# Performance work log

Hardware: AMD Instinct MI355X
Metric: run time of the kernel (lower is better)

## Reference

```python
import jax, jax.numpy as jnp
import numpy as np

B, S, H = 2, 2048, 1024
NH = 16
HD = H // NH


def setup_inputs() -> dict:
    key = jax.random.key(0)
    ks = jax.random.split(key, 5)
    X = jax.random.normal(ks[0], (B, S, H), dtype=jnp.float32)
    mask = jnp.ones((B, S), dtype=jnp.int32)
    W_Q = jax.random.normal(ks[1], (H, H), dtype=jnp.float32) * 0.02
    W_K = jax.random.normal(ks[2], (H, H), dtype=jnp.float32) * 0.02
    W_V = jax.random.normal(ks[3], (H, H), dtype=jnp.float32) * 0.02
    W_O = jax.random.normal(ks[4], (H, H), dtype=jnp.float32) * 0.02
    return {"X": X, "mask": mask, "W_Q": W_Q, "W_K": W_K, "W_V": W_V, "W_O": W_O}


def reference(X, mask, W_Q, W_K, W_V, W_O):
    b, s, h = X.shape
    scaling = HD ** -0.5
    # project and split heads: [b, nh, s, hd]
    Q = (X @ W_Q).reshape(b, s, NH, HD).transpose(0, 2, 1, 3)
    K = (X @ W_K).reshape(b, s, NH, HD).transpose(0, 2, 1, 3)
    V = (X @ W_V).reshape(b, s, NH, HD).transpose(0, 2, 1, 3)
    scores = jnp.einsum('bhqd,bhkd->bhqk', Q, K) * scaling
    scores = jnp.clip(scores, -10000.0, 10000.0)
    # 2D mask [b, s] -> broadcast as [b, 1, 1, s]; fill -inf where mask == 0
    m = mask[:, None, None, :]
    scores = jnp.where(m == 0, -jnp.inf, scores)
    attn = jax.nn.softmax(scores, axis=-1)
    # dropout is identity in eval / p=0
    context = jnp.einsum('bhqk,bhkd->bhqd', attn, V)
    context = context.transpose(0, 2, 1, 3).reshape(b, s, h)
    return context @ W_O
```

## Files before the change

### kernel.cpp

```cpp
#include <hip/hip_runtime.h>
#include <hip/hip_bf16.h>

#define S_LEN 2048
#define HDIM  1024
#define NHEADS 16
#define HD    64
#define QKV_STRIDE (S_LEN * 2 * HDIM)

typedef __attribute__((ext_vector_type(8))) short short8;
typedef __attribute__((ext_vector_type(4))) float float4v;

__device__ __forceinline__ unsigned short f2bf(float f) {
  return (unsigned short)((__builtin_bit_cast(unsigned int, f) + 0x8000u) >> 16);
}
__device__ __forceinline__ unsigned int pkbf(float a, float b) {
  unsigned int ua = __builtin_bit_cast(unsigned int, a) + 0x8000u;
  unsigned int ub = __builtin_bit_cast(unsigned int, b) + 0x8000u;
  return __builtin_amdgcn_perm(ub, ua, 0x07060302u);
}

__device__ __forceinline__ void async_copy16(const void* g, void* l) {
  __builtin_amdgcn_global_load_lds((__attribute__((address_space(1))) const void*)g,
                                   (__attribute__((address_space(3))) void*)l, 16, 0, 0);
}

__global__ void cast_x_kernel(const float* __restrict__ X, unsigned short* __restrict__ Xb) {
  int i = blockIdx.x * blockDim.x + threadIdx.x;
  float4 v = ((const float4*)X)[i];
  uint2 o;
  o.x = pkbf(v.x, v.y);
  o.y = pkbf(v.z, v.w);
  ((uint2*)Xb)[i] = o;
}

__global__ void trans_w_kernel(const float* __restrict__ W0, const float* __restrict__ W1,
                               const float* __restrict__ W2, const float* __restrict__ W3,
                               unsigned short* __restrict__ Wt) {
  __shared__ unsigned short tile[64][72];
  const float* W = (blockIdx.z == 0) ? W0 : (blockIdx.z == 1) ? W1 : (blockIdx.z == 2) ? W2 : W3;
  unsigned short* out = Wt + (size_t)blockIdx.z * HDIM * HDIM;
  int n0 = blockIdx.x * 64, k0 = blockIdx.y * 64;
  int t = threadIdx.x;
#pragma unroll
  for (int it = 0; it < 4; ++it) {
    int idx = it * 256 + t;
    int r  = idx >> 4;
    int c4 = (idx & 15) * 4;
    float4 v = *(const float4*)&W[(size_t)(k0 + r) * HDIM + n0 + c4];
    tile[c4 + 0][r] = f2bf(v.x);
    tile[c4 + 1][r] = f2bf(v.y);
    tile[c4 + 2][r] = f2bf(v.z);
    tile[c4 + 3][r] = f2bf(v.w);
  }
  __syncthreads();
#pragma unroll
  for (int it = 0; it < 4; ++it) {
    int idx = it * 256 + t;
    int r  = idx >> 4;
    int c4 = (idx & 15) * 4;
    ushort4 o;
    o.x = tile[r][c4 + 0]; o.y = tile[r][c4 + 1];
    o.z = tile[r][c4 + 2]; o.w = tile[r][c4 + 3];
    *(ushort4*)&out[(size_t)(n0 + r) * HDIM + k0 + c4] = o;
  }
}

__global__ __launch_bounds__(256, 3) void gemm128_kernel(
    const unsigned short* __restrict__ A,
    const unsigned short* __restrict__ B0, const unsigned short* __restrict__ B1,
    const unsigned short* __restrict__ B2,
    void* __restrict__ outp, int mode)
{
  __shared__ unsigned short sA[128 * 32];
  __shared__ unsigned short sB[128 * 32];
  const int z = blockIdx.z;
  const unsigned short* Bt = (z == 0) ? B0 : (z == 1) ? B1 : B2;
  const int m0 = blockIdx.x * 128;
  const int n0 = blockIdx.y * 128;
  const int t = threadIdx.x;
  const int lane = t & 63;
  const int w = t >> 6;
  const int wm = w & 1, wn = w >> 1;

  const int sr  = lane >> 2;
  const int scp = lane & 3;
  const int scl = scp ^ ((sr >> 1) & 3);
  const long ga0 = (long)(m0 + 16 * w + sr) * HDIM + scl * 8;
  const long ga1 = ga0 + 64l * HDIM;
  const long gb0 = (long)(n0 + 16 * w + sr) * HDIM + scl * 8;
  const long gb1 = gb0 + 64l * HDIM;
  unsigned short* lA0 = &sA[(16 * w) * 32];
  unsigned short* lA1 = &sA[(64 + 16 * w) * 32];
  unsigned short* lB0 = &sB[(16 * w) * 32];
  unsigned short* lB1 = &sB[(64 + 16 * w) * 32];

  const int fr = lane & 15;
  const int fq = lane >> 4;
  int offA[4], offB[4];
#pragma unroll
  for (int i = 0; i < 4; ++i) {
    int ra = wm * 64 + i * 16 + fr;
    offA[i] = ra * 32 + (fq ^ ((ra >> 1) & 3)) * 8;
    int rb = wn * 64 + i * 16 + fr;
    offB[i] = rb * 32 + (fq ^ ((rb >> 1) & 3)) * 8;
  }

  float4v acc[4][4] = {};

  for (int kk = 0; kk < HDIM; kk += 32) {
    __syncthreads();
    async_copy16(A + ga0 + kk, lA0);
    async_copy16(A + ga1 + kk, lA1);
    async_copy16(Bt + gb0 + kk, lB0);
    async_copy16(Bt + gb1 + kk, lB1);
    __syncthreads();
    short8 af[4], bf[4];
#pragma unroll
    for (int i = 0; i < 4; ++i) af[i] = *(const short8*)&sA[offA[i]];
#pragma unroll
    for (int i = 0; i < 4; ++i) bf[i] = *(const short8*)&sB[offB[i]];
#pragma unroll
    for (int mi = 0; mi < 4; ++mi)
#pragma unroll
      for (int ni = 0; ni < 4; ++ni)
        acc[mi][ni] = __builtin_amdgcn_mfma_f32_16x16x32_bf16(af[mi], bf[ni], acc[mi][ni], 0, 0, 0);
  }

  if (mode == 0) {
    float* out = (float*)outp;
#pragma unroll
    for (int mi = 0; mi < 4; ++mi)
#pragma unroll
      for (int ni = 0; ni < 4; ++ni)
#pragma unroll
        for (int rg = 0; rg < 4; ++rg) {
          int m = m0 + wm * 64 + mi * 16 + fq * 4 + rg;
          int n = n0 + wn * 64 + ni * 16 + fr;
          out[(size_t)m * HDIM + n] = acc[mi][ni][rg];
        }
  } else if (z != 1) {
    const float scl = (z == 0) ? 0.18033688011112042f : 1.0f;
    unsigned short* out = (unsigned short*)outp + (size_t)z * QKV_STRIDE;
#pragma unroll
    for (int mi = 0; mi < 4; ++mi)
#pragma unroll
      for (int ni = 0; ni < 4; ++ni) {
        int m = m0 + wm * 64 + mi * 16 + fq * 4;
        int n = n0 + wn * 64 + ni * 16 + fr;
        int b = m >> 11, s = m & 2047, hh = n >> 6, d = n & 63;
        uint2 pk;
        pk.x = pkbf(acc[mi][ni][0] * scl, acc[mi][ni][1] * scl);
        pk.y = pkbf(acc[mi][ni][2] * scl, acc[mi][ni][3] * scl);
        *(uint2*)&out[(((size_t)(b * NHEADS + hh)) * HD + d) * S_LEN + s] = pk;
      }
  } else {
    unsigned short* out = (unsigned short*)outp + (size_t)z * QKV_STRIDE;
#pragma unroll
    for (int mi = 0; mi < 4; ++mi)
#pragma unroll
      for (int ni = 0; ni < 4; ++ni)
#pragma unroll
        for (int rg = 0; rg < 4; ++rg) {
          int m = m0 + wm * 64 + mi * 16 + fq * 4 + rg;
          int n = n0 + wn * 64 + ni * 16 + fr;
          int b = m >> 11, s = m & 2047, hh = n >> 6, d = n & 63;
          out[(((size_t)(b * NHEADS + hh)) * S_LEN + s) * HD + d] = f2bf(acc[mi][ni][rg]);
        }
  }
}

__device__ __forceinline__ void stage_tile(char* smem, const unsigned short* Kp,
    const unsigned short* Vtp, size_t base, int tile, int w, int kr, int kc) {
  const int kv = tile * 64;
  char* bufb = smem + (tile & 1) * 16384;
  unsigned short* dK = (unsigned short*)bufb + (w * 8) * 64;
  async_copy16(Kp + base + (size_t)(kv + w * 8 + kr) * HD + ((kc ^ kr) * 8), dK);
  unsigned short* dV = (unsigned short*)(bufb + 8192) + (w * 8) * 64;
  const int d = w * 8 + kr;
  async_copy16(Vtp + base + (size_t)d * S_LEN + kv + ((kc ^ kr) * 8), dV);
}

__global__ __launch_bounds__(512, 4) void attn_kernel(
    const unsigned short* __restrict__ Qtp,
    const unsigned short* __restrict__ Kp,
    const unsigned short* __restrict__ Vtp,
    const int* __restrict__ mask,
    unsigned short* __restrict__ ctx)
{
  __shared__ __align__(16) char smem[53248];

  const int bh = blockIdx.y;
  const int b = bh >> 4;
  const int h = bh & 15;
  const size_t base = (size_t)bh * (S_LEN * HD);
  const int q0 = blockIdx.x * 128;
  const int t = threadIdx.x;
  const int lane = t & 63;
  const int w = t >> 6;
  const int qg = w >> 1;
  const int kh = w & 1;
  const int fr = lane & 15;
  const int fq = lane >> 4;
  const int kr = lane >> 3, kc = lane & 7;
  unsigned short* sPw = (unsigned short*)(smem + 32768) + w * (32 * 40);

  short8 qfr[2][2];
#pragma unroll
  for (int q_ = 0; q_ < 2; ++q_)
#pragma unroll
    for (int ks = 0; ks < 2; ++ks)
#pragma unroll
      for (int j = 0; j < 8; ++j)
        qfr[q_][ks][j] = (short)Qtp[base + (size_t)(ks * 32 + fq * 8 + j) * S_LEN
                                    + (q0 + qg * 32 + q_ * 16 + fr)];

  float l_lane[2] = {0.f, 0.f};
  float4v o_acc[4][2] = {};
  const float4v zero4 = {0.f, 0.f, 0.f, 0.f};

  int mnext = mask[b * S_LEN + lane];

  stage_tile(smem, Kp, Vtp, base, 0, w, kr, kc);

#pragma unroll 2
  for (int it = 0; it < 32; ++it) {
    __syncthreads();
    if (it < 31)
      stage_tile(smem, Kp, Vtp, base, it + 1, w, kr, kc);

    unsigned long long bal = __ballot(mnext != 0);
    if (it < 31)
      mnext = mask[b * S_LEN + (it + 1) * 64 + lane];

    const unsigned short* sKb  = (const unsigned short*)(smem + (it & 1) * 16384);
    const unsigned short* sVtb = (const unsigned short*)(smem + (it & 1) * 16384 + 8192);

    float4v s_acc[2][2];
#pragma unroll
    for (int kf = 0; kf < 2; ++kf) {
      int rk = kh * 32 + kf * 16 + fr;
      short8 k0 = *(const short8*)&sKb[rk * 64 + ((fq ^ (rk & 7)) * 8)];
      short8 k1 = *(const short8*)&sKb[rk * 64 + (((4 + fq) ^ (rk & 7)) * 8)];
#pragma unroll
      for (int q_ = 0; q_ < 2; ++q_) {
        float4v s = __builtin_amdgcn_mfma_f32_16x16x32_bf16(k0, qfr[q_][0], zero4, 0, 0, 0);
        s_acc[kf][q_] = __builtin_amdgcn_mfma_f32_16x16x32_bf16(k1, qfr[q_][1], s, 0, 0, 0);
      }
    }

    short8 vf[4];
#pragma unroll
    for (int df = 0; df < 4; ++df) {
      int rv = df * 16 + fr;
      vf[df] = *(const short8*)&sVtb[rv * 64 + (((kh * 4 + fq) ^ (fr & 7)) * 8)];
    }

#pragma unroll
    for (int kf = 0; kf < 2; ++kf) {
      unsigned mseg = 0xFu;
      if (bal != ~0ull)
        mseg = (unsigned)(bal >> (kh * 32 + kf * 16 + fq * 4)) & 0xFu;
#pragma unroll
      for (int q_ = 0; q_ < 2; ++q_) {
        float p0 = __builtin_amdgcn_exp2f(s_acc[kf][q_][0]);
        float p1 = __builtin_amdgcn_exp2f(s_acc[kf][q_][1]);
        float p2 = __builtin_amdgcn_exp2f(s_acc[kf][q_][2]);
        float p3 = __builtin_amdgcn_exp2f(s_acc[kf][q_][3]);
        if (bal != ~0ull) {
          p0 = (mseg & 1u) ? p0 : 0.f;
          p1 = (mseg & 2u) ? p1 : 0.f;
          p2 = (mseg & 4u) ? p2 : 0.f;
          p3 = (mseg & 8u) ? p3 : 0.f;
        }
        l_lane[q_] += (p0 + p1) + (p2 + p3);
        uint2 pk;
        pk.x = pkbf(p0, p1);
        pk.y = pkbf(p2, p3);
        *(uint2*)&sPw[(q_ * 16 + fr) * 40 + (kf * 4 + fq) * 4] = pk;
      }
    }

    short8 pf[2];
#pragma unroll
    for (int q_ = 0; q_ < 2; ++q_)
      pf[q_] = *(const short8*)&sPw[(q_ * 16 + fr) * 40 + fq * 8];
#pragma unroll
    for (int df = 0; df < 4; ++df)
#pragma unroll
      for (int q_ = 0; q_ < 2; ++q_)
        o_acc[df][q_] = __builtin_amdgcn_mfma_f32_16x16x32_bf16(vf[df], pf[q_], o_acc[df][q_], 0, 0, 0);
  }

#pragma unroll
  for (int q_ = 0; q_ < 2; ++q_) {
    l_lane[q_] += __shfl_xor(l_lane[q_], 16);
    l_lane[q_] += __shfl_xor(l_lane[q_], 32);
  }

  __syncthreads();
  float* red = (float*)smem;
  float* rec = red + (size_t)(qg * 64 + lane) * 34;
  if (kh) {
#pragma unroll
    for (int df = 0; df < 4; ++df)
#pragma unroll
      for (int q_ = 0; q_ < 2; ++q_) {
        int e = df * 2 + q_;
        *(float2*)&rec[4 * e]     = make_float2(o_acc[df][q_][0], o_acc[df][q_][1]);
        *(float2*)&rec[4 * e + 2] = make_float2(o_acc[df][q_][2], o_acc[df][q_][3]);
      }
    *(float2*)&rec[32] = make_float2(l_lane[0], l_lane[1]);
  }
  __syncthreads();
  if (!kh) {
#pragma unroll
    for (int df = 0; df < 4; ++df)
#pragma unroll
      for (int q_ = 0; q_ < 2; ++q_) {
        int e = df * 2 + q_;
        float2 a = *(float2*)&rec[4 * e];
        float2 c = *(float2*)&rec[4 * e + 2];
        o_acc[df][q_][0] += a.x; o_acc[df][q_][1] += a.y;
        o_acc[df][q_][2] += c.x; o_acc[df][q_][3] += c.y;
      }
    float2 lr = *(float2*)&rec[32];
    float inv_l[2];
    inv_l[0] = 1.0f / (l_lane[0] + lr.x);
    inv_l[1] = 1.0f / (l_lane[1] + lr.y);
#pragma unroll
    for (int q_ = 0; q_ < 2; ++q_) {
      size_t rowoff = ((size_t)(b * S_LEN + q0 + qg * 32 + q_ * 16 + fr)) * HDIM + h * HD;
#pragma unroll
      for (int df = 0; df < 4; ++df) {
        uint2 pk;
        pk.x = pkbf(o_acc[df][q_][0] * inv_l[q_], o_acc[df][q_][1] * inv_l[q_]);
        pk.y = pkbf(o_acc[df][q_][2] * inv_l[q_], o_acc[df][q_][3] * inv_l[q_]);
        *(uint2*)&ctx[rowoff + df * 16 + fq * 4] = pk;
      }
    }
  }
}

extern "C" void kernel_launch(void* const* d_in, const int* in_sizes, int n_in,
                              void* d_out, int out_size, void* d_ws, size_t ws_size,
                              hipStream_t stream) {
  const float* X  = (const float*)d_in[0];
  const int* mask = (const int*)d_in[1];
  const float* Wq = (const float*)d_in[2];
  const float* Wk = (const float*)d_in[3];
  const float* Wv = (const float*)d_in[4];
  const float* Wo = (const float*)d_in[5];
  float* out = (float*)d_out;

  char* ws = (char*)d_ws;
  unsigned short* Xb  = (unsigned short*)(ws);
  unsigned short* Wt  = (unsigned short*)(ws + (8u << 20));
  unsigned short* QKV = (unsigned short*)(ws + (16u << 20));
  unsigned short* CTX = (unsigned short*)(ws);

  cast_x_kernel<<<4096, 256, 0, stream>>>(X, Xb);
  trans_w_kernel<<<dim3(16, 16, 4), 256, 0, stream>>>(Wq, Wk, Wv, Wo, Wt);
  gemm128_kernel<<<dim3(32, 8, 3), 256, 0, stream>>>(
      Xb, Wt, Wt + (1u << 20), Wt + (2u << 20), QKV, 1);
  attn_kernel<<<dim3(16, 32), 512, 0, stream>>>(
      QKV, QKV + QKV_STRIDE, QKV + 2 * (size_t)QKV_STRIDE, mask, CTX);
  gemm128_kernel<<<dim3(32, 8, 1), 256, 0, stream>>>(
      CTX, Wt + (3u << 20), Wt + (3u << 20), Wt + (3u << 20), out, 0);
}
```

Measured before the change: 187.2 us.

## Merge prep kernels and fuse QKV projections into one shared-A GEMM

Folds the X cast and weight transpose into a single prep launch, removing one kernel launch. Replaces the three-way z-indexed QKV GEMM with one kernel in which each block computes a 128x64 tile for Q, K and V together. This reuses each A tile from LDS across all three weights, cutting A loads threefold. It also simplifies the output GEMM by dropping its mode branches. The cost is more accumulator registers (96 floats per lane), occupancy lowered to 2 blocks, and a grid that shrinks to 512 blocks.

```diff
diff --git a/kernel.cpp b/kernel.cpp
--- a/kernel.cpp
+++ b/kernel.cpp
@@ -24,23 +24,28 @@
                                    (__attribute__((address_space(3))) void*)l, 16, 0, 0);
 }
 
-__global__ void cast_x_kernel(const float* __restrict__ X, unsigned short* __restrict__ Xb) {
-  int i = blockIdx.x * blockDim.x + threadIdx.x;
-  float4 v = ((const float4*)X)[i];
-  uint2 o;
-  o.x = pkbf(v.x, v.y);
-  o.y = pkbf(v.z, v.w);
-  ((uint2*)Xb)[i] = o;
-}
-
-__global__ void trans_w_kernel(const float* __restrict__ W0, const float* __restrict__ W1,
-                               const float* __restrict__ W2, const float* __restrict__ W3,
-                               unsigned short* __restrict__ Wt) {
+__global__ void prep_kernel(const float* __restrict__ X, unsigned short* __restrict__ Xb,
+                            const float* __restrict__ W0, const float* __restrict__ W1,
+                            const float* __restrict__ W2, const float* __restrict__ W3,
+                            unsigned short* __restrict__ Wt) {
   __shared__ unsigned short tile[64][72];
-  const float* W = (blockIdx.z == 0) ? W0 : (blockIdx.z == 1) ? W1 : (blockIdx.z == 2) ? W2 : W3;
-  unsigned short* out = Wt + (size_t)blockIdx.z * HDIM * HDIM;
-  int n0 = blockIdx.x * 64, k0 = blockIdx.y * 64;
-  int t = threadIdx.x;
+  const int t = threadIdx.x;
+  if (blockIdx.x < 4096) {
+    int i = blockIdx.x * 256 + t;
+    float4 v = ((const float4*)X)[i];
+    uint2 o;
+    o.x = pkbf(v.x, v.y);
+    o.y = pkbf(v.z, v.w);
+    ((uint2*)Xb)[i] = o;
+    return;
+  }
+  const int wid = blockIdx.x - 4096;
+  const int z = wid >> 8;
+  const int rem = wid & 255;
+  const int n0 = (rem & 15) * 64;
+  const int k0 = (rem >> 4) * 64;
+  const float* W = (z == 0) ? W0 : (z == 1) ? W1 : (z == 2) ? W2 : W3;
+  unsigned short* out = Wt + (size_t)z * HDIM * HDIM;
 #pragma unroll
   for (int it = 0; it < 4; ++it) {
     int idx = it * 256 + t;
@@ -65,16 +70,109 @@
   }
 }
 
+__global__ __launch_bounds__(256, 2) void gemm_qkv_kernel(
+    const unsigned short* __restrict__ A,
+    const unsigned short* __restrict__ Wt,
+    unsigned short* __restrict__ out)
+{
+  __shared__ unsigned short sA[128 * 32];
+  __shared__ unsigned short sB[3 * 64 * 32];
+  const int m0 = blockIdx.x * 128;
+  const int n0 = blockIdx.y * 64;
+  const int t = threadIdx.x;
+  const int lane = t & 63;
+  const int w = t >> 6;
+  const int wm = w & 1, wn = w >> 1;
+
+  const int sr  = lane >> 2;
+  const int scp = lane & 3;
+  const int scl = scp ^ ((sr >> 1) & 3);
+  const long ga0 = (long)(m0 + 16 * w + sr) * HDIM + scl * 8;
+  const long ga1 = ga0 + 64l * HDIM;
+  const long gb  = (long)(n0 + 16 * w + sr) * HDIM + scl * 8;
+  unsigned short* lA0 = &sA[(16 * w) * 32];
+  unsigned short* lA1 = &sA[(64 + 16 * w) * 32];
+  unsigned short* lB  = &sB[(16 * w) * 32];
+
+  const int fr = lane & 15;
+  const int fq = lane >> 4;
+  int offA[4], offB[2];
+#pragma unroll
+  for (int i = 0; i < 4; ++i) {
+    int ra = wm * 64 + i * 16 + fr;
+    offA[i] = ra * 32 + (fq ^ ((ra >> 1) & 3)) * 8;
+  }
+#pragma unroll
+  for (int i = 0; i < 2; ++i) {
+    int rb = wn * 32 + i * 16 + fr;
+    offB[i] = rb * 32 + (fq ^ ((rb >> 1) & 3)) * 8;
+  }
+
+  float4v acc[3][4][2] = {};
+
+  for (int kk = 0; kk < HDIM; kk += 32) {
+    __syncthreads();
+    async_copy16(A + ga0 + kk, lA0);
+    async_copy16(A + ga1 + kk, lA1);
+#pragma unroll
+    for (int z = 0; z < 3; ++z)
+      async_copy16(Wt + (long)z * (HDIM * HDIM) + gb + kk, lB + z * 2048);
+    __syncthreads();
+    short8 af[4];
+#pragma unroll
+    for (int i = 0; i < 4; ++i) af[i] = *(const short8*)&sA[offA[i]];
+#pragma unroll
+    for (int z = 0; z < 3; ++z) {
+      short8 b0 = *(const short8*)&sB[z * 2048 + offB[0]];
+      short8 b1 = *(const short8*)&sB[z * 2048 + offB[1]];
+#pragma unroll
+      for (int mi = 0; mi < 4; ++mi) {
+        acc[z][mi][0] = __builtin_amdgcn_mfma_f32_16x16x32_bf16(af[mi], b0, acc[z][mi][0], 0, 0, 0);
+        acc[z][mi][1] = __builtin_amdgcn_mfma_f32_16x16x32_bf16(af[mi], b1, acc[z][mi][1], 0, 0, 0);
+      }
+    }
+  }
+
+#pragma unroll
+  for (int z = 0; z < 3; z += 2) {
+    const float scle = (z == 0) ? 0.18033688011112042f : 1.0f;
+    unsigned short* o = out + (size_t)z * QKV_STRIDE;
+#pragma unroll
+    for (int mi = 0; mi < 4; ++mi)
+#pragma unroll
+      for (int ni = 0; ni < 2; ++ni) {
+        int m = m0 + wm * 64 + mi * 16 + fq * 4;
+        int n = n0 + wn * 32 + ni * 16 + fr;
+        int b = m >> 11, s = m & 2047, hh = n >> 6, d = n & 63;
+        uint2 pk;
+        pk.x = pkbf(acc[z][mi][ni][0] * scle, acc[z][mi][ni][1] * scle);
+        pk.y = pkbf(acc[z][mi][ni][2] * scle, acc[z][mi][ni][3] * scle);
+        *(uint2*)&o[(((size_t)(b * NHEADS + hh)) * HD + d) * S_LEN + s] = pk;
+      }
+  }
+  {
+    unsigned short* o = out + (size_t)QKV_STRIDE;
+#pragma unroll
+    for (int mi = 0; mi < 4; ++mi)
+#pragma unroll
+      for (int ni = 0; ni < 2; ++ni)
+#pragma unroll
+        for (int rg = 0; rg < 4; ++rg) {
+          int m = m0 + wm * 64 + mi * 16 + fq * 4 + rg;
+          int n = n0 + wn * 32 + ni * 16 + fr;
+          int b = m >> 11, s = m & 2047, hh = n >> 6, d = n & 63;
+          o[(((size_t)(b * NHEADS + hh)) * S_LEN + s) * HD + d] = f2bf(acc[1][mi][ni][rg]);
+        }
+  }
+}
+
 __global__ __launch_bounds__(256, 3) void gemm128_kernel(
     const unsigned short* __restrict__ A,
-    const unsigned short* __restrict__ B0, const unsigned short* __restrict__ B1,
-    const unsigned short* __restrict__ B2,
-    void* __restrict__ outp, int mode)
+    const unsigned short* __restrict__ Bt,
+    float* __restrict__ out)
 {
   __shared__ unsigned short sA[128 * 32];
   __shared__ unsigned short sB[128 * 32];
-  const int z = blockIdx.z;
-  const unsigned short* Bt = (z == 0) ? B0 : (z == 1) ? B1 : B2;
   const int m0 = blockIdx.x * 128;
   const int n0 = blockIdx.y * 128;
   const int t = threadIdx.x;
@@ -126,47 +224,16 @@
         acc[mi][ni] = __builtin_amdgcn_mfma_f32_16x16x32_bf16(af[mi], bf[ni], acc[mi][ni], 0, 0, 0);
   }
 
-  if (mode == 0) {
-    float* out = (float*)outp;
-#pragma unroll
-    for (int mi = 0; mi < 4; ++mi)
-#pragma unroll
-      for (int ni = 0; ni < 4; ++ni)
-#pragma unroll
-        for (int rg = 0; rg < 4; ++rg) {
-          int m = m0 + wm * 64 + mi * 16 + fq * 4 + rg;
-          int n = n0 + wn * 64 + ni * 16 + fr;
-          out[(size_t)m * HDIM + n] = acc[mi][ni][rg];
-        }
-  } else if (z != 1) {
-    const float scl = (z == 0) ? 0.18033688011112042f : 1.0f;
-    unsigned short* out = (unsigned short*)outp + (size_t)z * QKV_STRIDE;
-#pragma unroll
-    for (int mi = 0; mi < 4; ++mi)
-#pragma unroll
-      for (int ni = 0; ni < 4; ++ni) {
-        int m = m0 + wm * 64 + mi * 16 + fq * 4;
+#pragma unroll
+  for (int mi = 0; mi < 4; ++mi)
+#pragma unroll
+    for (int ni = 0; ni < 4; ++ni)
+#pragma unroll
+      for (int rg = 0; rg < 4; ++rg) {
+        int m = m0 + wm * 64 + mi * 16 + fq * 4 + rg;
         int n = n0 + wn * 64 + ni * 16 + fr;
-        int b = m >> 11, s = m & 2047, hh = n >> 6, d = n & 63;
-        uint2 pk;
-        pk.x = pkbf(acc[mi][ni][0] * scl, acc[mi][ni][1] * scl);
-        pk.y = pkbf(acc[mi][ni][2] * scl, acc[mi][ni][3] * scl);
-        *(uint2*)&out[(((size_t)(b * NHEADS + hh)) * HD + d) * S_LEN + s] = pk;
-      }
-  } else {
-    unsigned short* out = (unsigned short*)outp + (size_t)z * QKV_STRIDE;
-#pragma unroll
-    for (int mi = 0; mi < 4; ++mi)
-#pragma unroll
-      for (int ni = 0; ni < 4; ++ni)
-#pragma unroll
-        for (int rg = 0; rg < 4; ++rg) {
-          int m = m0 + wm * 64 + mi * 16 + fq * 4 + rg;
-          int n = n0 + wn * 64 + ni * 16 + fr;
-          int b = m >> 11, s = m & 2047, hh = n >> 6, d = n & 63;
-          out[(((size_t)(b * NHEADS + hh)) * S_LEN + s) * HD + d] = f2bf(acc[mi][ni][rg]);
-        }
-  }
+        out[(size_t)m * HDIM + n] = acc[mi][ni][rg];
+      }
 }
 
 __device__ __forceinline__ void stage_tile(char* smem, const unsigned short* Kp,
@@ -358,12 +425,9 @@
   unsigned short* QKV = (unsigned short*)(ws + (16u << 20));
   unsigned short* CTX = (unsigned short*)(ws);
 
-  cast_x_kernel<<<4096, 256, 0, stream>>>(X, Xb);
-  trans_w_kernel<<<dim3(16, 16, 4), 256, 0, stream>>>(Wq, Wk, Wv, Wo, Wt);
-  gemm128_kernel<<<dim3(32, 8, 3), 256, 0, stream>>>(
-      Xb, Wt, Wt + (1u << 20), Wt + (2u << 20), QKV, 1);
+  prep_kernel<<<5120, 256, 0, stream>>>(X, Xb, Wq, Wk, Wv, Wo, Wt);
+  gemm_qkv_kernel<<<dim3(32, 16), 256, 0, stream>>>(Xb, Wt, QKV);
   attn_kernel<<<dim3(16, 32), 512, 0, stream>>>(
       QKV, QKV + QKV_STRIDE, QKV + 2 * (size_t)QKV_STRIDE, mask, CTX);
-  gemm128_kernel<<<dim3(32, 8, 1), 256, 0, stream>>>(
-      CTX, Wt + (3u << 20), Wt + (3u << 20), Wt + (3u << 20), out, 0);
-}
+  gemm128_kernel<<<dim3(32, 8), 256, 0, stream>>>(CTX, Wt + (3u << 20), out);
+}
```

New measurement: 187.6 us. No clear change (+0.2%).
